# Kernel tuning notes

Hardware: AMD Instinct MI355X
Metric: run time of the kernel (lower is better)

Reference implementation:

```python
import jax, jax.numpy as jnp
import numpy as np

B, T, C, H = 2, 2048, 1024, 16
D = C // H  # head_dim = 64

def setup_inputs() -> dict:
    key = jax.random.key(0)
    ks = jax.random.split(key, 5)
    x = jax.random.normal(ks[0], (B, T, C), dtype=jnp.float32)
    # additive causal mask, broadcastable to (B, H, T, T)
    neg = jnp.float32(-1e9)
    causal = jnp.tril(jnp.ones((T, T), dtype=bool))
    attention_mask = jnp.where(causal, 0.0, neg)[None, None, :, :]
    scale = 0.02
    W_attn = jax.random.normal(ks[1], (C, 3 * C), dtype=jnp.float32) * scale
    b_attn = jnp.zeros((3 * C,), dtype=jnp.float32)
    W_proj = jax.random.normal(ks[2], (C, C), dtype=jnp.float32) * scale
    b_proj = jnp.zeros((C,), dtype=jnp.float32)
    return {"x": x, "attention_mask": attention_mask, "W_attn": W_attn,
            "b_attn": b_attn, "W_proj": W_proj, "b_proj": b_proj}

def reference(x, attention_mask, W_attn, b_attn, W_proj, b_proj):
    b, t, c = x.shape
    qkv = x @ W_attn + b_attn                       # (B,T,3C)
    q, k, v = jnp.split(qkv, 3, axis=-1)
    # (B,T,C) -> (B,H,T,D)
    def heads(u):
        return u.reshape(b, t, H, D).transpose(0, 2, 1, 3)
    q, k, v = heads(q), heads(k), heads(v)
    att = jnp.einsum("bhqd,bhkd->bhqk", q, k) * (1.0 / np.sqrt(D))
    att = att + attention_mask
    att_weights = jax.nn.softmax(att, axis=-1)      # (B,H,T,T)
    y = jnp.einsum("bhqk,bhkd->bhqd", att_weights, v)
    y = y.transpose(0, 2, 1, 3).reshape(b, t, c)    # (B,T,C)
    y = y @ W_proj + b_proj
    return (y, att_weights)
```

## Files before the change

kernel.cpp:

```cpp
#include <hip/hip_runtime.h>
#include <hip/hip_bf16.h>

#define B_ 2
#define T_ 2048
#define C_ 1024
#define H_ 16
#define D_ 64
#define BT_ (B_*T_)
#define N3_ (3*C_)
#define NQT_ (T_/64)

typedef float f32x4 __attribute__((ext_vector_type(4)));
typedef unsigned short u16x8 __attribute__((ext_vector_type(8)));
typedef __bf16 bf16x8 __attribute__((ext_vector_type(8)));

__device__ __forceinline__ f32x4 mfma16(u16x8 a, u16x8 b, f32x4 c) {
  union Cvt { u16x8 u; bf16x8 h; };
  Cvt ua, ub; ua.u = a; ub.u = b;
  return __builtin_amdgcn_mfma_f32_16x16x32_bf16(ua.h, ub.h, c, 0, 0, 0);
}

__device__ __forceinline__ unsigned short f2bf(float f) {
  union { float f; unsigned u; } v; v.f = f;
  unsigned r = v.u + 0x7FFFu + ((v.u >> 16) & 1u);
  return (unsigned short)(r >> 16);
}

__device__ __forceinline__ float bf2f(unsigned short u) {
  union { unsigned u; float f; } v; v.u = ((unsigned)u) << 16;
  return v.f;
}

__device__ __forceinline__ void gload_lds16(const unsigned short* g, unsigned short* l) {
  __builtin_amdgcn_global_load_lds(
      (const __attribute__((address_space(1))) unsigned int*)g,
      (__attribute__((address_space(3))) unsigned int*)l, 16, 0, 0);
}

__global__ __launch_bounds__(256) void transpose_to_bf16T(
    const float* __restrict__ W, unsigned short* __restrict__ WT, int K, int N) {
  __shared__ float tile[32][33];
  int n0 = blockIdx.x * 32, k0 = blockIdx.y * 32;
  int tx = threadIdx.x & 31, ty = threadIdx.x >> 5;
#pragma unroll
  for (int i = 0; i < 4; ++i)
    tile[ty + i * 8][tx] = W[(size_t)(k0 + ty + i * 8) * N + n0 + tx];
  __syncthreads();
#pragma unroll
  for (int i = 0; i < 4; ++i)
    WT[(size_t)(n0 + ty + i * 8) * K + k0 + tx] = f2bf(tile[tx][ty + i * 8]);
}

__global__ __launch_bounds__(256) void convert_x(const float* __restrict__ x,
                                                 unsigned short* __restrict__ xb) {
  int i = (blockIdx.x * 256 + threadIdx.x) * 8;
  f32x4 a = *(const f32x4*)(x + i);
  f32x4 b = *(const f32x4*)(x + i + 4);
  u16x8 o;
  o[0]=f2bf(a[0]); o[1]=f2bf(a[1]); o[2]=f2bf(a[2]); o[3]=f2bf(a[3]);
  o[4]=f2bf(b[0]); o[5]=f2bf(b[1]); o[6]=f2bf(b[2]); o[7]=f2bf(b[3]);
  *(u16x8*)(xb + i) = o;
}

__global__ __launch_bounds__(256) void gemm_qkv(
    const unsigned short* __restrict__ xb, const unsigned short* __restrict__ WaT,
    const float* __restrict__ bias, unsigned short* __restrict__ qkv) {
  __shared__ __attribute__((aligned(16))) unsigned short As[128 * 32];
  __shared__ __attribute__((aligned(16))) unsigned short Bs[128 * 32];
  int n0 = blockIdx.x * 128;
  int m0 = blockIdx.y * 128;
  int tid = threadIdx.x;
  int lane = tid & 63, wid = tid >> 6;
  int wm = wid >> 1, wn = wid & 1;
  int l15 = lane & 15, l4 = lane >> 4;
  int srow = lane >> 2, scol = (lane & 3) << 3;

  f32x4 acc[4][4];
#pragma unroll
  for (int i = 0; i < 4; ++i)
#pragma unroll
    for (int j = 0; j < 4; ++j) acc[i][j] = (f32x4){0.f, 0.f, 0.f, 0.f};

  for (int ks = 0; ks < C_ / 32; ++ks) {
#pragma unroll
    for (int j = 0; j < 2; ++j) {
      int row = wid * 16 + j * 64 + srow;
      gload_lds16(xb + (size_t)(m0 + row) * C_ + ks * 32 + scol,
                  &As[(wid * 16 + j * 64) * 32]);
      gload_lds16(WaT + (size_t)(n0 + row) * C_ + ks * 32 + scol,
                  &Bs[(wid * 16 + j * 64) * 32]);
    }
    __syncthreads();
    u16x8 af[4], bfr[4];
#pragma unroll
    for (int mi = 0; mi < 4; ++mi)
      af[mi] = *(const u16x8*)&As[(wm * 64 + mi * 16 + l15) * 32 + l4 * 8];
#pragma unroll
    for (int ni = 0; ni < 4; ++ni)
      bfr[ni] = *(const u16x8*)&Bs[(wn * 64 + ni * 16 + l15) * 32 + l4 * 8];
#pragma unroll
    for (int mi = 0; mi < 4; ++mi)
#pragma unroll
      for (int ni = 0; ni < 4; ++ni) acc[mi][ni] = mfma16(af[mi], bfr[ni], acc[mi][ni]);
    __syncthreads();
  }
#pragma unroll
  for (int mi = 0; mi < 4; ++mi)
#pragma unroll
    for (int ni = 0; ni < 4; ++ni)
#pragma unroll
      for (int rr = 0; rr < 4; ++rr) {
        int m = m0 + wm * 64 + mi * 16 + l4 * 4 + rr;
        int n = n0 + wn * 64 + ni * 16 + l15;
        float v = acc[mi][ni][rr] + bias[n];
        int b = m >> 11, tok = m & (T_ - 1);
        int sect = n >> 10, h = (n >> 6) & 15, d = n & 63;
        size_t idx;
        if (sect < 2)
          idx = ((((size_t)sect * B_ + b) * H_ + h) * T_ + tok) * D_ + d;
        else
          idx = (size_t)2 * B_ * H_ * T_ * D_ + (((size_t)b * H_ + h) * D_ + d) * T_ + tok;
        qkv[idx] = f2bf(v);
      }
}

__global__ __launch_bounds__(256) void attn_kernel(
    const unsigned short* __restrict__ qkv, float* __restrict__ att,
    unsigned short* __restrict__ Y) {
  int qpair = blockIdx.x;
  int h = blockIdx.y;
  int b = blockIdx.z;
  int tid = threadIdx.x, lane = tid & 63, wid = tid >> 6;
  int l15 = lane & 15, l4 = lane >> 4;

  const unsigned short* Q = qkv + (((size_t)(0 * B_ + b) * H_ + h) * T_) * D_;
  const unsigned short* K = qkv + (((size_t)(1 * B_ + b) * H_ + h) * T_) * D_;
  const unsigned short* VtG = qkv + (size_t)2 * B_ * H_ * T_ * D_ +
                              (((size_t)b * H_ + h) * D_) * T_;
  float* attbase = att + ((size_t)(b * H_ + h) * T_) * T_;

  __shared__ __attribute__((aligned(16))) unsigned short Ps[64][72];
  __shared__ __attribute__((aligned(16))) unsigned short Vt[64][72];

  const float scale = 0.125f;

  for (int qsel = 0; qsel < 2; ++qsel) {
    int qt = qsel ? (NQT_ - 1 - qpair) : qpair;
    int q0 = qt * 64;

    u16x8 qf[2];
#pragma unroll
    for (int c = 0; c < 2; ++c)
      qf[c] = *(const u16x8*)(Q + (size_t)(q0 + wid * 16 + l15) * D_ + c * 32 + l4 * 8);

    int myrow[4];
#pragma unroll
    for (int rr = 0; rr < 4; ++rr) myrow[rr] = q0 + wid * 16 + l4 * 4 + rr;

    float esum[4] = {0.f, 0.f, 0.f, 0.f};
    for (int kt = 0; kt <= qt; ++kt) {
      int k0 = kt * 64;
      f32x4 s[4];
#pragma unroll
      for (int g = 0; g < 4; ++g) s[g] = (f32x4){0.f, 0.f, 0.f, 0.f};
#pragma unroll
      for (int g = 0; g < 4; ++g)
#pragma unroll
        for (int c = 0; c < 2; ++c) {
          u16x8 kf = *(const u16x8*)(K + (size_t)(k0 + g * 16 + l15) * D_ + c * 32 + l4 * 8);
          s[g] = mfma16(qf[c], kf, s[g]);
        }
      bool diag = (kt == qt);
#pragma unroll
      for (int g = 0; g < 4; ++g) {
        int col = k0 + g * 16 + l15;
#pragma unroll
        for (int rr = 0; rr < 4; ++rr) {
          float p = (diag && col > myrow[rr]) ? 0.f : __expf(s[g][rr] * scale);
          esum[rr] += p;
        }
      }
    }
    float inv_l[4];
#pragma unroll
    for (int rr = 0; rr < 4; ++rr) {
      float e = esum[rr];
      e += __shfl_xor(e, 1);
      e += __shfl_xor(e, 2);
      e += __shfl_xor(e, 4);
      e += __shfl_xor(e, 8);
      inv_l[rr] = 1.f / e;
    }

    f32x4 yacc[4];
#pragma unroll
    for (int g = 0; g < 4; ++g) yacc[g] = (f32x4){0.f, 0.f, 0.f, 0.f};

    for (int kt = 0; kt <= qt; ++kt) {
      int k0 = kt * 64;
      __syncthreads();
      {
        int dd = tid >> 2;
        int kq = (tid & 3) * 16;
        const unsigned short* vsrc = VtG + (size_t)dd * T_ + k0 + kq;
        u16x8 v0 = *(const u16x8*)(vsrc);
        u16x8 v1 = *(const u16x8*)(vsrc + 8);
        *(u16x8*)&Vt[dd][kq] = v0;
        *(u16x8*)&Vt[dd][kq + 8] = v1;
      }
      f32x4 s[4];
#pragma unroll
      for (int g = 0; g < 4; ++g) s[g] = (f32x4){0.f, 0.f, 0.f, 0.f};
#pragma unroll
      for (int g = 0; g < 4; ++g)
#pragma unroll
        for (int c = 0; c < 2; ++c) {
          u16x8 kf = *(const u16x8*)(K + (size_t)(k0 + g * 16 + l15) * D_ + c * 32 + l4 * 8);
          s[g] = mfma16(qf[c], kf, s[g]);
        }
      bool diag = (kt == qt);
#pragma unroll
      for (int g = 0; g < 4; ++g) {
        int col = k0 + g * 16 + l15;
#pragma unroll
        for (int rr = 0; rr < 4; ++rr) {
          float p = (diag && col > myrow[rr]) ? 0.f
                                              : __expf(s[g][rr] * scale) * inv_l[rr];
          Ps[wid * 16 + l4 * 4 + rr][g * 16 + l15] = f2bf(p);
        }
      }
      {
        int cc = l15 * 4;
#pragma unroll
        for (int jj = 0; jj < 4; ++jj) {
          int rrow = wid * 16 + jj * 4 + l4;
          const unsigned short* ps = &Ps[rrow][cc];
          f32x4 o;
          o[0] = bf2f(ps[0]); o[1] = bf2f(ps[1]);
          o[2] = bf2f(ps[2]); o[3] = bf2f(ps[3]);
          *(f32x4*)&attbase[(size_t)(q0 + rrow) * T_ + k0 + cc] = o;
        }
      }
      __syncthreads();
#pragma unroll
      for (int c = 0; c < 2; ++c) {
        u16x8 pf = *(const u16x8*)&Ps[wid * 16 + l15][c * 32 + l4 * 8];
#pragma unroll
        for (int g = 0; g < 4; ++g) {
          u16x8 vf = *(const u16x8*)&Vt[g * 16 + l15][c * 32 + l4 * 8];
          yacc[g] = mfma16(pf, vf, yacc[g]);
        }
      }
    }

    f32x4 z = (f32x4){0.f, 0.f, 0.f, 0.f};
    for (int kt = qt + 1; kt < NQT_; ++kt) {
      int k0 = kt * 64;
#pragma unroll
      for (int rr = 0; rr < 4; ++rr)
        *(f32x4*)&attbase[(size_t)myrow[rr] * T_ + k0 + l15 * 4] = z;
    }

#pragma unroll
    for (int g = 0; g < 4; ++g)
#pragma unroll
      for (int rr = 0; rr < 4; ++rr)
        Y[(size_t)(b * T_ + myrow[rr]) * C_ + h * D_ + g * 16 + l15] = f2bf(yacc[g][rr]);

    __syncthreads();
  }
}

__global__ __launch_bounds__(256) void gemm_proj(
    const unsigned short* __restrict__ Y, const unsigned short* __restrict__ WpT,
    const float* __restrict__ bias, float* __restrict__ out) {
  __shared__ __attribute__((aligned(16))) unsigned short As[128 * 32];
  __shared__ __attribute__((aligned(16))) unsigned short Bs[128 * 32];
  int n0 = blockIdx.x * 128;
  int m0 = blockIdx.y * 128;
  int tid = threadIdx.x;
  int lane = tid & 63, wid = tid >> 6;
  int wm = wid >> 1, wn = wid & 1;
  int l15 = lane & 15, l4 = lane >> 4;
  int srow = lane >> 2, scol = (lane & 3) << 3;

  f32x4 acc[4][4];
#pragma unroll
  for (int i = 0; i < 4; ++i)
#pragma unroll
    for (int j = 0; j < 4; ++j) acc[i][j] = (f32x4){0.f, 0.f, 0.f, 0.f};

  for (int ks = 0; ks < C_ / 32; ++ks) {
#pragma unroll
    for (int j = 0; j < 2; ++j) {
      int row = wid * 16 + j * 64 + srow;
      gload_lds16(Y + (size_t)(m0 + row) * C_ + ks * 32 + scol,
                  &As[(wid * 16 + j * 64) * 32]);
      gload_lds16(WpT + (size_t)(n0 + row) * C_ + ks * 32 + scol,
                  &Bs[(wid * 16 + j * 64) * 32]);
    }
    __syncthreads();
    u16x8 af[4], bfr[4];
#pragma unroll
    for (int mi = 0; mi < 4; ++mi)
      af[mi] = *(const u16x8*)&As[(wm * 64 + mi * 16 + l15) * 32 + l4 * 8];
#pragma unroll
    for (int ni = 0; ni < 4; ++ni)
      bfr[ni] = *(const u16x8*)&Bs[(wn * 64 + ni * 16 + l15) * 32 + l4 * 8];
#pragma unroll
    for (int mi = 0; mi < 4; ++mi)
#pragma unroll
      for (int ni = 0; ni < 4; ++ni) acc[mi][ni] = mfma16(af[mi], bfr[ni], acc[mi][ni]);
    __syncthreads();
  }
#pragma unroll
  for (int mi = 0; mi < 4; ++mi)
#pragma unroll
    for (int ni = 0; ni < 4; ++ni)
#pragma unroll
      for (int rr = 0; rr < 4; ++rr) {
        int m = m0 + wm * 64 + mi * 16 + l4 * 4 + rr;
        int n = n0 + wn * 64 + ni * 16 + l15;
        out[(size_t)m * C_ + n] = acc[mi][ni][rr] + bias[n];
      }
}

extern "C" void kernel_launch(void* const* d_in, const int* in_sizes, int n_in,
                              void* d_out, int out_size, void* d_ws, size_t ws_size,
                              hipStream_t stream) {
  const float* x = (const float*)d_in[0];
  const float* W_attn = (const float*)d_in[2];
  const float* b_attn = (const float*)d_in[3];
  const float* W_proj = (const float*)d_in[4];
  const float* b_proj = (const float*)d_in[5];

  float* out_y = (float*)d_out;
  float* out_att = (float*)d_out + (size_t)BT_ * C_;

  unsigned short* WaT = (unsigned short*)d_ws;
  unsigned short* WpT = WaT + (size_t)N3_ * C_;
  unsigned short* qkvb = WpT + (size_t)C_ * C_;
  unsigned short* Yb = qkvb + (size_t)3 * B_ * H_ * T_ * D_;
  unsigned short* xb = Yb + (size_t)BT_ * C_;

  transpose_to_bf16T<<<dim3(N3_ / 32, C_ / 32), 256, 0, stream>>>(W_attn, WaT, C_, N3_);
  transpose_to_bf16T<<<dim3(C_ / 32, C_ / 32), 256, 0, stream>>>(W_proj, WpT, C_, C_);
  convert_x<<<dim3(BT_ * C_ / (256 * 8)), 256, 0, stream>>>(x, xb);
  gemm_qkv<<<dim3(N3_ / 128, BT_ / 128), 256, 0, stream>>>(xb, WaT, b_attn, qkvb);
  attn_kernel<<<dim3(NQT_ / 2, H_, B_), 256, 0, stream>>>(qkvb, out_att, Yb);
  gemm_proj<<<dim3(C_ / 128, BT_ / 128), 256, 0, stream>>>(Yb, WpT, b_proj, out_y);
}
```

Baseline: 304.4 us.

## Stage V-transpose epilogue through LDS and split attention into per-tile blocks

In the QKV GEMM, the V section's transposed output is now written by staging the tile in shared memory and issuing coalesced 16-byte stores, instead of scattered 2-byte stores along the token stride. The attention kernel drops the paired-query-tile loop and launches one block per (q-tile, head, batch), ordered longest-first, so there are more blocks and the scheduler balances the causal work. The attention-weight writes now come from the register fragment already loaded for the PV MFMA, which removes a separate shared-memory readback. Costs are extra LDS traffic and barriers in the GEMM epilogue, and relying on hardware block scheduling instead of manual pairing for load balance.

```diff
diff --git a/kernel.cpp b/kernel.cpp
--- a/kernel.cpp
+++ b/kernel.cpp
@@ -65,8 +65,9 @@
 __global__ __launch_bounds__(256) void gemm_qkv(
     const unsigned short* __restrict__ xb, const unsigned short* __restrict__ WaT,
     const float* __restrict__ bias, unsigned short* __restrict__ qkv) {
-  __shared__ __attribute__((aligned(16))) unsigned short As[128 * 32];
-  __shared__ __attribute__((aligned(16))) unsigned short Bs[128 * 32];
+  __shared__ __attribute__((aligned(16))) unsigned short S[2][128 * 32];
+  unsigned short* As = S[0];
+  unsigned short* Bs = S[1];
   int n0 = blockIdx.x * 128;
   int m0 = blockIdx.y * 128;
   int tid = threadIdx.x;
@@ -104,32 +105,66 @@
       for (int ni = 0; ni < 4; ++ni) acc[mi][ni] = mfma16(af[mi], bfr[ni], acc[mi][ni]);
     __syncthreads();
   }
-#pragma unroll
-  for (int mi = 0; mi < 4; ++mi)
-#pragma unroll
-    for (int ni = 0; ni < 4; ++ni)
-#pragma unroll
-      for (int rr = 0; rr < 4; ++rr) {
-        int m = m0 + wm * 64 + mi * 16 + l4 * 4 + rr;
+
+  if (n0 < 2 * C_) {
+#pragma unroll
+    for (int mi = 0; mi < 4; ++mi)
+#pragma unroll
+      for (int ni = 0; ni < 4; ++ni)
+#pragma unroll
+        for (int rr = 0; rr < 4; ++rr) {
+          int m = m0 + wm * 64 + mi * 16 + l4 * 4 + rr;
+          int n = n0 + wn * 64 + ni * 16 + l15;
+          float v = acc[mi][ni][rr] + bias[n];
+          int b = m >> 11, tok = m & (T_ - 1);
+          int sect = n >> 10, h = (n >> 6) & 15, d = n & 63;
+          size_t idx = ((((size_t)sect * B_ + b) * H_ + h) * T_ + tok) * D_ + d;
+          qkv[idx] = f2bf(v);
+        }
+  } else {
+    unsigned short* L = S[0];
+    unsigned short* vbase = qkv + (size_t)2 * B_ * H_ * T_ * D_;
+    int bq = m0 >> 11, tok0 = m0 & (T_ - 1);
+#pragma unroll
+    for (int half = 0; half < 2; ++half) {
+#pragma unroll
+      for (int ni2 = 0; ni2 < 2; ++ni2) {
+        int ni = half * 2 + ni2;
+        int r = wn * 32 + ni2 * 16 + l15;
         int n = n0 + wn * 64 + ni * 16 + l15;
-        float v = acc[mi][ni][rr] + bias[n];
-        int b = m >> 11, tok = m & (T_ - 1);
-        int sect = n >> 10, h = (n >> 6) & 15, d = n & 63;
-        size_t idx;
-        if (sect < 2)
-          idx = ((((size_t)sect * B_ + b) * H_ + h) * T_ + tok) * D_ + d;
-        else
-          idx = (size_t)2 * B_ * H_ * T_ * D_ + (((size_t)b * H_ + h) * D_ + d) * T_ + tok;
-        qkv[idx] = f2bf(v);
-      }
+#pragma unroll
+        for (int mi = 0; mi < 4; ++mi)
+#pragma unroll
+          for (int rr = 0; rr < 4; ++rr) {
+            int mloc = wm * 64 + mi * 16 + l4 * 4 + rr;
+            L[r * 128 + mloc] = f2bf(acc[mi][ni][rr] + bias[n]);
+          }
+      }
+      __syncthreads();
+#pragma unroll
+      for (int pass = 0; pass < 4; ++pass) {
+        int r = pass * 16 + (tid >> 4);
+        int chunk = tid & 15;
+        int n_local = (r >> 5) * 64 + half * 32 + (r & 31);
+        int n = n0 + n_local;
+        int h = (n >> 6) & 15, d = n & 63;
+        u16x8 val = *(const u16x8*)&L[r * 128 + chunk * 8];
+        *(u16x8*)&vbase[(((size_t)bq * H_ + h) * D_ + d) * T_ + tok0 + chunk * 8] = val;
+      }
+      __syncthreads();
+    }
+  }
 }
 
 __global__ __launch_bounds__(256) void attn_kernel(
     const unsigned short* __restrict__ qkv, float* __restrict__ att,
     unsigned short* __restrict__ Y) {
-  int qpair = blockIdx.x;
-  int h = blockIdx.y;
-  int b = blockIdx.z;
+  int idx = blockIdx.x;
+  int qt = NQT_ - 1 - (idx >> 5);
+  int hb = idx & 31;
+  int h = hb & 15;
+  int b = hb >> 4;
+  int q0 = qt * 64;
   int tid = threadIdx.x, lane = tid & 63, wid = tid >> 6;
   int l15 = lane & 15, l4 = lane >> 4;
 
@@ -144,131 +179,121 @@
 
   const float scale = 0.125f;
 
-  for (int qsel = 0; qsel < 2; ++qsel) {
-    int qt = qsel ? (NQT_ - 1 - qpair) : qpair;
-    int q0 = qt * 64;
-
-    u16x8 qf[2];
-#pragma unroll
-    for (int c = 0; c < 2; ++c)
-      qf[c] = *(const u16x8*)(Q + (size_t)(q0 + wid * 16 + l15) * D_ + c * 32 + l4 * 8);
-
-    int myrow[4];
-#pragma unroll
-    for (int rr = 0; rr < 4; ++rr) myrow[rr] = q0 + wid * 16 + l4 * 4 + rr;
-
-    float esum[4] = {0.f, 0.f, 0.f, 0.f};
-    for (int kt = 0; kt <= qt; ++kt) {
-      int k0 = kt * 64;
-      f32x4 s[4];
-#pragma unroll
-      for (int g = 0; g < 4; ++g) s[g] = (f32x4){0.f, 0.f, 0.f, 0.f};
-#pragma unroll
-      for (int g = 0; g < 4; ++g)
-#pragma unroll
-        for (int c = 0; c < 2; ++c) {
-          u16x8 kf = *(const u16x8*)(K + (size_t)(k0 + g * 16 + l15) * D_ + c * 32 + l4 * 8);
-          s[g] = mfma16(qf[c], kf, s[g]);
-        }
-      bool diag = (kt == qt);
+  u16x8 qf[2];
+#pragma unroll
+  for (int c = 0; c < 2; ++c)
+    qf[c] = *(const u16x8*)(Q + (size_t)(q0 + wid * 16 + l15) * D_ + c * 32 + l4 * 8);
+
+  int myrow[4];
+#pragma unroll
+  for (int rr = 0; rr < 4; ++rr) myrow[rr] = q0 + wid * 16 + l4 * 4 + rr;
+
+  float esum[4] = {0.f, 0.f, 0.f, 0.f};
+  for (int kt = 0; kt <= qt; ++kt) {
+    int k0 = kt * 64;
+    f32x4 s[4];
+#pragma unroll
+    for (int g = 0; g < 4; ++g) s[g] = (f32x4){0.f, 0.f, 0.f, 0.f};
+#pragma unroll
+    for (int g = 0; g < 4; ++g)
+#pragma unroll
+      for (int c = 0; c < 2; ++c) {
+        u16x8 kf = *(const u16x8*)(K + (size_t)(k0 + g * 16 + l15) * D_ + c * 32 + l4 * 8);
+        s[g] = mfma16(qf[c], kf, s[g]);
+      }
+    bool diag = (kt == qt);
+#pragma unroll
+    for (int g = 0; g < 4; ++g) {
+      int col = k0 + g * 16 + l15;
+#pragma unroll
+      for (int rr = 0; rr < 4; ++rr) {
+        float p = (diag && col > myrow[rr]) ? 0.f : __expf(s[g][rr] * scale);
+        esum[rr] += p;
+      }
+    }
+  }
+  float inv_l[4];
+#pragma unroll
+  for (int rr = 0; rr < 4; ++rr) {
+    float e = esum[rr];
+    e += __shfl_xor(e, 1);
+    e += __shfl_xor(e, 2);
+    e += __shfl_xor(e, 4);
+    e += __shfl_xor(e, 8);
+    inv_l[rr] = 1.f / e;
+  }
+
+  f32x4 yacc[4];
+#pragma unroll
+  for (int g = 0; g < 4; ++g) yacc[g] = (f32x4){0.f, 0.f, 0.f, 0.f};
+
+  for (int kt = 0; kt <= qt; ++kt) {
+    int k0 = kt * 64;
+    __syncthreads();
+    {
+      int dd = tid >> 2;
+      int kq = (tid & 3) * 16;
+      const unsigned short* vsrc = VtG + (size_t)dd * T_ + k0 + kq;
+      u16x8 v0 = *(const u16x8*)(vsrc);
+      u16x8 v1 = *(const u16x8*)(vsrc + 8);
+      *(u16x8*)&Vt[dd][kq] = v0;
+      *(u16x8*)&Vt[dd][kq + 8] = v1;
+    }
+    f32x4 s[4];
+#pragma unroll
+    for (int g = 0; g < 4; ++g) s[g] = (f32x4){0.f, 0.f, 0.f, 0.f};
+#pragma unroll
+    for (int g = 0; g < 4; ++g)
+#pragma unroll
+      for (int c = 0; c < 2; ++c) {
+        u16x8 kf = *(const u16x8*)(K + (size_t)(k0 + g * 16 + l15) * D_ + c * 32 + l4 * 8);
+        s[g] = mfma16(qf[c], kf, s[g]);
+      }
+    bool diag = (kt == qt);
+#pragma unroll
+    for (int g = 0; g < 4; ++g) {
+      int col = k0 + g * 16 + l15;
+#pragma unroll
+      for (int rr = 0; rr < 4; ++rr) {
+        float p = (diag && col > myrow[rr]) ? 0.f
+                                            : __expf(s[g][rr] * scale) * inv_l[rr];
+        Ps[wid * 16 + l4 * 4 + rr][g * 16 + l15] = f2bf(p);
+      }
+    }
+    __syncthreads();
+#pragma unroll
+    for (int c = 0; c < 2; ++c) {
+      u16x8 pf = *(const u16x8*)&Ps[wid * 16 + l15][c * 32 + l4 * 8];
+      {
+        int arow = q0 + wid * 16 + l15;
+        float* dst = &attbase[(size_t)arow * T_ + k0 + c * 32 + l4 * 8];
+        f32x4 o0, o1;
+        o0[0] = bf2f(pf[0]); o0[1] = bf2f(pf[1]); o0[2] = bf2f(pf[2]); o0[3] = bf2f(pf[3]);
+        o1[0] = bf2f(pf[4]); o1[1] = bf2f(pf[5]); o1[2] = bf2f(pf[6]); o1[3] = bf2f(pf[7]);
+        *(f32x4*)(dst) = o0;
+        *(f32x4*)(dst + 4) = o1;
+      }
 #pragma unroll
       for (int g = 0; g < 4; ++g) {
-        int col = k0 + g * 16 + l15;
-#pragma unroll
-        for (int rr = 0; rr < 4; ++rr) {
-          float p = (diag && col > myrow[rr]) ? 0.f : __expf(s[g][rr] * scale);
-          esum[rr] += p;
-        }
-      }
-    }
-    float inv_l[4];
-#pragma unroll
-    for (int rr = 0; rr < 4; ++rr) {
-      float e = esum[rr];
-      e += __shfl_xor(e, 1);
-      e += __shfl_xor(e, 2);
-      e += __shfl_xor(e, 4);
-      e += __shfl_xor(e, 8);
-      inv_l[rr] = 1.f / e;
-    }
-
-    f32x4 yacc[4];
-#pragma unroll
-    for (int g = 0; g < 4; ++g) yacc[g] = (f32x4){0.f, 0.f, 0.f, 0.f};
-
-    for (int kt = 0; kt <= qt; ++kt) {
-      int k0 = kt * 64;
-      __syncthreads();
-      {
-        int dd = tid >> 2;
-        int kq = (tid & 3) * 16;
-        const unsigned short* vsrc = VtG + (size_t)dd * T_ + k0 + kq;
-        u16x8 v0 = *(const u16x8*)(vsrc);
-        u16x8 v1 = *(const u16x8*)(vsrc + 8);
-        *(u16x8*)&Vt[dd][kq] = v0;
-        *(u16x8*)&Vt[dd][kq + 8] = v1;
-      }
-      f32x4 s[4];
-#pragma unroll
-      for (int g = 0; g < 4; ++g) s[g] = (f32x4){0.f, 0.f, 0.f, 0.f};
-#pragma unroll
-      for (int g = 0; g < 4; ++g)
-#pragma unroll
-        for (int c = 0; c < 2; ++c) {
-          u16x8 kf = *(const u16x8*)(K + (size_t)(k0 + g * 16 + l15) * D_ + c * 32 + l4 * 8);
-          s[g] = mfma16(qf[c], kf, s[g]);
-        }
-      bool diag = (kt == qt);
-#pragma unroll
-      for (int g = 0; g < 4; ++g) {
-        int col = k0 + g * 16 + l15;
-#pragma unroll
-        for (int rr = 0; rr < 4; ++rr) {
-          float p = (diag && col > myrow[rr]) ? 0.f
-                                              : __expf(s[g][rr] * scale) * inv_l[rr];
-          Ps[wid * 16 + l4 * 4 + rr][g * 16 + l15] = f2bf(p);
-        }
-      }
-      {
-        int cc = l15 * 4;
-#pragma unroll
-        for (int jj = 0; jj < 4; ++jj) {
-          int rrow = wid * 16 + jj * 4 + l4;
-          const unsigned short* ps = &Ps[rrow][cc];
-          f32x4 o;
-          o[0] = bf2f(ps[0]); o[1] = bf2f(ps[1]);
-          o[2] = bf2f(ps[2]); o[3] = bf2f(ps[3]);
-          *(f32x4*)&attbase[(size_t)(q0 + rrow) * T_ + k0 + cc] = o;
-        }
-      }
-      __syncthreads();
-#pragma unroll
-      for (int c = 0; c < 2; ++c) {
-        u16x8 pf = *(const u16x8*)&Ps[wid * 16 + l15][c * 32 + l4 * 8];
-#pragma unroll
-        for (int g = 0; g < 4; ++g) {
-          u16x8 vf = *(const u16x8*)&Vt[g * 16 + l15][c * 32 + l4 * 8];
-          yacc[g] = mfma16(pf, vf, yacc[g]);
-        }
-      }
-    }
-
-    f32x4 z = (f32x4){0.f, 0.f, 0.f, 0.f};
-    for (int kt = qt + 1; kt < NQT_; ++kt) {
-      int k0 = kt * 64;
-#pragma unroll
-      for (int rr = 0; rr < 4; ++rr)
-        *(f32x4*)&attbase[(size_t)myrow[rr] * T_ + k0 + l15 * 4] = z;
-    }
-
-#pragma unroll
-    for (int g = 0; g < 4; ++g)
-#pragma unroll
-      for (int rr = 0; rr < 4; ++rr)
-        Y[(size_t)(b * T_ + myrow[rr]) * C_ + h * D_ + g * 16 + l15] = f2bf(yacc[g][rr]);
-
-    __syncthreads();
-  }
+        u16x8 vf = *(const u16x8*)&Vt[g * 16 + l15][c * 32 + l4 * 8];
+        yacc[g] = mfma16(pf, vf, yacc[g]);
+      }
+    }
+  }
+
+  f32x4 z = (f32x4){0.f, 0.f, 0.f, 0.f};
+  for (int kt = qt + 1; kt < NQT_; ++kt) {
+    int k0 = kt * 64;
+#pragma unroll
+    for (int rr = 0; rr < 4; ++rr)
+      *(f32x4*)&attbase[(size_t)myrow[rr] * T_ + k0 + l15 * 4] = z;
+  }
+
+#pragma unroll
+  for (int g = 0; g < 4; ++g)
+#pragma unroll
+    for (int rr = 0; rr < 4; ++rr)
+      Y[(size_t)(b * T_ + myrow[rr]) * C_ + h * D_ + g * 16 + l15] = f2bf(yacc[g][rr]);
 }
 
 __global__ __launch_bounds__(256) void gemm_proj(
@@ -347,6 +372,6 @@
   transpose_to_bf16T<<<dim3(C_ / 32, C_ / 32), 256, 0, stream>>>(W_proj, WpT, C_, C_);
   convert_x<<<dim3(BT_ * C_ / (256 * 8)), 256, 0, stream>>>(x, xb);
   gemm_qkv<<<dim3(N3_ / 128, BT_ / 128), 256, 0, stream>>>(xb, WaT, b_attn, qkvb);
-  attn_kernel<<<dim3(NQT_ / 2, H_, B_), 256, 0, stream>>>(qkvb, out_att, Yb);
+  attn_kernel<<<dim3(NQT_ * H_ * B_), 256, 0, stream>>>(qkvb, out_att, Yb);
   gemm_proj<<<dim3(C_ / 128, BT_ / 128), 256, 0, stream>>>(Yb, WpT, b_proj, out_y);
 }
```

Result: slower. 319.7 us (+5.0%).
